# Optimization experiments

Hardware: AMD Instinct MI355X
Metric: run time of the kernel (lower is better)

The kernel has to match this reference:

```python
import jax, jax.numpy as jnp
import numpy as np

B, Nq, C, H = 1, 300, 256, 8
h, w = 32, 32
HW = h * w
HID = 512  # rpe_hidden_dim
HD = C // H


def setup_inputs() -> dict:
    key = jax.random.key(0)
    ks = jax.random.split(key, 16)
    s = 0.02
    inp = {
        "raw_query": jax.random.normal(ks[0], (B, Nq, C), jnp.float32),
        "query_pos": jax.random.normal(ks[1], (B, Nq, C), jnp.float32),
        "reference_points": jax.random.uniform(ks[2], (B, Nq, 2), jnp.float32),
        "raw_src": jax.random.normal(ks[3], (B, HW, C), jnp.float32),
        "src_pos_embed": jax.random.normal(ks[4], (B, HW, C), jnp.float32),
        "Wq": jax.random.normal(ks[5], (C, C), jnp.float32) * s,
        "bq": jnp.zeros((C,), jnp.float32),
        "Wk": jax.random.normal(ks[6], (C, C), jnp.float32) * s,
        "bk": jnp.zeros((C,), jnp.float32),
        "Wv": jax.random.normal(ks[7], (C, C), jnp.float32) * s,
        "bv": jnp.zeros((C,), jnp.float32),
        "Wo": jax.random.normal(ks[8], (C, C), jnp.float32) * s,
        "bo": jnp.zeros((C,), jnp.float32),
        "W1": jax.random.normal(ks[9], (HID, 2), jnp.float32),   # cpb MLP layer 1
        "b1": jnp.zeros((HID,), jnp.float32),
        "W2": jax.random.normal(ks[10], (H, HID), jnp.float32) * s,  # cpb MLP layer 2 (no bias)
        "input_spatial_shapes": np.array([[h, w]], dtype=np.int64),
    }
    return inp


def _key_positions(hh, ww):
    ys = (jnp.arange(hh, dtype=jnp.float32) + 0.5) / hh
    xs = (jnp.arange(ww, dtype=jnp.float32) + 0.5) / ww
    yy, xx = jnp.meshgrid(ys, xs, indexing="ij")  # row-major: idx = y*w + x
    return jnp.stack([xx.ravel(), yy.ravel()], axis=-1)  # [HW, 2] (x, y)


def reference(raw_query, query_pos, reference_points, raw_src, src_pos_embed,
              Wq, bq, Wk, bk, Wv, bv, Wo, bo, W1, b1, W2, input_spatial_shapes):
    hh, ww = int(input_spatial_shapes[0, 0]), int(input_spatial_shapes[0, 1])
    scale = HD ** (-0.5)
    queries = raw_query + query_pos                      # [B,Nq,C]
    memory = raw_src + src_pos_embed                     # [B,HW,C]

    q = (queries @ Wq.T + bq).reshape(B, Nq, H, HD)
    k = (memory @ Wk.T + bk).reshape(B, hh * ww, H, HD)
    v = (memory @ Wv.T + bv).reshape(B, hh * ww, H, HD)

    logits = jnp.einsum("bqhd,bkhd->bhqk", q, k) * scale  # [B,H,Nq,HW]

    key_pos = _key_positions(hh, ww)                      # [HW,2]
    delta = reference_points[:, :, None, :] - key_pos[None, None]  # [B,Nq,HW,2]
    hid = jax.nn.relu(jnp.einsum("bqkc,hc->bqkh", delta, W1) + b1)  # [B,Nq,HW,HID]
    bias = jnp.einsum("bqkf,hf->bhqk", hid, W2)           # [B,H,Nq,HW]

    attn = jax.nn.softmax(logits + bias, axis=-1)
    out = jnp.einsum("bhqk,bkhd->bqhd", attn, v).reshape(B, Nq, C)
    return out @ Wo.T + bo
```

## Files before the change

### kernel.cpp

```cpp
#include <hip/hip_runtime.h>
#include <hip/hip_bf16.h>
#include <stdint.h>

#define NQ   300
#define CDIM 256
#define NH   8
#define HD   32
#define HWK  1024
#define HIDD 512

typedef __attribute__((ext_vector_type(8))) short short8;
typedef __attribute__((ext_vector_type(4))) float f32x4;

#define QB_OFF   0
#define KB_OFF   153600
#define VT_OFF   677888
#define PO_OFF   1202176
#define PL_OFF   2430976

__device__ __forceinline__ short sw_bf16(float x){
  union { float f; uint32_t u; } c; c.f = x;
  uint32_t u = c.u;
  u += 0x7fffu + ((u >> 16) & 1u);
  return (short)(u >> 16);
}

__device__ __forceinline__ uint32_t pk_bf16(float a, float b){
  __hip_bfloat162 h = __float22bfloat162_rn(make_float2(a, b));
  uint32_t u; __builtin_memcpy(&u, &h, 4);
  return u;
}

__global__ __launch_bounds__(256) void proj_kernel(
    const float* __restrict__ rq, const float* __restrict__ qp,
    const float* __restrict__ rs, const float* __restrict__ spe,
    const float* __restrict__ Wq, const float* __restrict__ bq,
    const float* __restrict__ Wk, const float* __restrict__ bk,
    const float* __restrict__ Wv, const float* __restrict__ bv,
    const float* __restrict__ Wo, const float* __restrict__ bo,
    char* __restrict__ ws, float* __restrict__ dout, int final_mode)
{
  int bxid = blockIdx.x;
  int tile = bxid >> 1, half = bxid & 1;
  const float *in1, *in2, *W, *bias;
  int r0, M, mode;
  const float* po = (const float*)(ws + PO_OFF);
  const float* pl = (const float*)(ws + PL_OFF);
  if (final_mode){
    in1 = po; in2 = nullptr; W = Wo; bias = bo;
    r0 = tile*16; M = NQ; mode = 3;
  } else if (tile < 19){
    in1 = rq; in2 = qp; W = Wq; bias = bq; r0 = tile*16; M = NQ; mode = 0;
  } else if (tile < 83){
    in1 = rs; in2 = spe; W = Wk; bias = bk; r0 = (tile-19)*16; M = HWK; mode = 1;
  } else {
    in1 = rs; in2 = spe; W = Wv; bias = bv; r0 = (tile-83)*16; M = HWK; mode = 2;
  }
  __shared__ __align__(16) float At[32][20];
  __shared__ float Wl[32][129];
  __shared__ float linv[16][8];
  int tid = threadIdx.x;
  int n_loc = tid & 127;
  int rg = tid >> 7;
  int n = half*128 + n_loc;
  float acc[8];
  float bv_ = bias[n];
  #pragma unroll
  for (int i=0;i<8;i++) acc[i] = bv_;

  if (mode == 3 && tid < 128){
    int r = tid >> 3, hh = tid & 7;
    int gr = r0 + r; if (gr >= M) gr = M - 1;
    float s = pl[(0*NQ+gr)*NH+hh] + pl[(1*NQ+gr)*NH+hh]
            + pl[(2*NQ+gr)*NH+hh] + pl[(3*NQ+gr)*NH+hh];
    linv[r][hh] = 1.0f / s;
  }

  for (int c0 = 0; c0 < CDIM; c0 += 32){
    __syncthreads();
    for (int e = tid; e < 512; e += 256){
      int r = e >> 5, c = e & 31;
      int gr = r0 + r; if (gr >= M) gr = M - 1;
      float v;
      if (mode == 3){
        int cc = c0 + c;
        v = po[(size_t)(0*NQ+gr)*CDIM + cc] + po[(size_t)(1*NQ+gr)*CDIM + cc]
          + po[(size_t)(2*NQ+gr)*CDIM + cc] + po[(size_t)(3*NQ+gr)*CDIM + cc];
        v *= linv[r][c0 >> 5];
      } else {
        v = in1[gr*CDIM + c0 + c];
        if (in2) v += in2[gr*CDIM + c0 + c];
      }
      At[c][r] = v;
    }
    for (int e = tid; e < 4096; e += 256){
      int c = e & 31, nn = e >> 5;
      Wl[c][nn] = W[(half*128 + nn)*CDIM + c0 + c];
    }
    __syncthreads();
    #pragma unroll
    for (int c = 0; c < 32; c++){
      float w = Wl[c][n_loc];
      const float4* ap = (const float4*)&At[c][rg*8];
      float4 a0 = ap[0], a1 = ap[1];
      acc[0] = fmaf(a0.x, w, acc[0]);
      acc[1] = fmaf(a0.y, w, acc[1]);
      acc[2] = fmaf(a0.z, w, acc[2]);
      acc[3] = fmaf(a0.w, w, acc[3]);
      acc[4] = fmaf(a1.x, w, acc[4]);
      acc[5] = fmaf(a1.y, w, acc[5]);
      acc[6] = fmaf(a1.z, w, acc[6]);
      acc[7] = fmaf(a1.w, w, acc[7]);
    }
  }

  if (mode == 0){
    short* qb = (short*)(ws + QB_OFF);
    const float s = 0.17677669529663687f;
    #pragma unroll
    for (int i=0;i<8;i++){
      int gr = r0 + rg*8 + i;
      if (gr < M) qb[gr*CDIM + n] = sw_bf16(acc[i]*s);
    }
  } else if (mode == 1){
    short* kb = (short*)(ws + KB_OFF);
    int h = n >> 5, d = n & 31;
    #pragma unroll
    for (int i=0;i<8;i++){
      int gr = r0 + rg*8 + i;
      if (gr < M) kb[((size_t)h*HWK + gr)*HD + d] = sw_bf16(acc[i]);
    }
  } else if (mode == 2){
    short* vt = (short*)(ws + VT_OFF);
    union { short8 s; uint32_t u[4]; } p;
    #pragma unroll
    for (int i=0;i<4;i++) p.u[i] = pk_bf16(acc[2*i], acc[2*i+1]);
    *(short8*)(vt + n*HWK + r0 + rg*8) = p.s;
  } else {
    #pragma unroll
    for (int i=0;i<8;i++){
      int gr = r0 + rg*8 + i;
      if (gr < M) dout[gr*CDIM + n] = acc[i];
    }
  }
}

__global__ __launch_bounds__(256) void fused_kernel(
    const float* __restrict__ refp, const float* __restrict__ W1,
    const float* __restrict__ b1, const float* __restrict__ W2,
    const short* __restrict__ qb, const short* __restrict__ kb,
    const short* __restrict__ vt, float* __restrict__ po,
    float* __restrict__ pl)
{
  int bid = blockIdx.x;
  int q = bid >> 2, kr = bid & 3;
  int tid = threadIdx.x, wave = tid >> 6, lane = tid & 63;
  int n = lane & 15, qd = lane >> 4;

  __shared__ __align__(16) float av[HIDD];
  __shared__ __align__(16) float wxs[HIDD];
  __shared__ __align__(16) float wys[HIDD];
  __shared__ __align__(16) short w2l[NH][520];
  __shared__ __align__(16) short pb[NH][264];
  __shared__ __align__(16) float part[4][NH][32];
  __shared__ float lsum[4][NH];

  float rx = refp[2*q], ry = refp[2*q+1];
  for (int f = tid; f < HIDD; f += 256){
    float2 w = ((const float2*)W1)[f];
    wxs[f] = w.x; wys[f] = w.y;
    av[f] = fmaf(w.x, rx, fmaf(w.y, ry, b1[f]));
  }
  for (int e = tid; e < 512; e += 256){
    int r = e >> 6, oc = e & 63;
    const float4* p4 = (const float4*)(W2 + r*HIDD + oc*8);
    float4 x0 = p4[0], x1 = p4[1];
    union { short8 s; uint32_t u[4]; } t;
    t.u[0] = pk_bf16(x0.x, x0.y);
    t.u[1] = pk_bf16(x0.z, x0.w);
    t.u[2] = pk_bf16(x1.x, x1.y);
    t.u[3] = pk_bf16(x1.z, x1.w);
    *(short8*)&w2l[r][oc*8] = t.s;
  }
  short8 qfrag;
  if (n < NH) qfrag = *(const short8*)(qb + q*CDIM + n*HD + qd*8);
  else { short8 z = {0,0,0,0,0,0,0,0}; qfrag = z; }
  __syncthreads();

  const int kbase = kr*256 + wave*64;

  f32x4 acc[4];
  #pragma unroll
  for (int t = 0; t < 4; t++){
    int k0 = kbase + t*16;
    f32x4 sel = {0.f,0.f,0.f,0.f};
    #pragma unroll
    for (int h = 0; h < NH; h++){
      short8 af = *(const short8*)(kb + ((size_t)h*HWK + k0 + n)*HD + qd*8);
      f32x4 d = {0.f,0.f,0.f,0.f};
      d = __builtin_amdgcn_mfma_f32_16x16x32_bf16(af, qfrag, d, 0, 0, 0);
      if (n == h) sel = d;
    }
    acc[t] = sel;
  }

  float kxA = ((float)n + 0.5f) * (1.0f/32.0f);
  float kxB = ((float)n + 16.5f) * (1.0f/32.0f);
  float kyA = ((float)(kbase >> 5) + 0.5f) * (1.0f/32.0f);
  float kyB = kyA + (1.0f/32.0f);
  #pragma unroll 2
  for (int kc = 0; kc < 16; kc++){
    int f0 = kc*32 + qd*8;
    f32x4 a0  = *(const f32x4*)&av[f0],  a1  = *(const f32x4*)&av[f0+4];
    f32x4 wx0 = *(const f32x4*)&wxs[f0], wx1 = *(const f32x4*)&wxs[f0+4];
    f32x4 wy0 = *(const f32x4*)&wys[f0], wy1 = *(const f32x4*)&wys[f0+4];
    short8 bfr = *(const short8*)&w2l[n & 7][kc*32 + qd*8];
    f32x4 tA0, tA1, tB0, tB1;
    #pragma unroll
    for (int j = 0; j < 4; j++){
      tA0[j] = fmaf(-wy0[j], kyA, a0[j]);
      tA1[j] = fmaf(-wy1[j], kyA, a1[j]);
      tB0[j] = fmaf(-wy0[j], kyB, a0[j]);
      tB1[j] = fmaf(-wy1[j], kyB, a1[j]);
    }
    #pragma unroll
    for (int t = 0; t < 4; t++){
      const f32x4& u0 = (t < 2) ? tA0 : tB0;
      const f32x4& u1 = (t < 2) ? tA1 : tB1;
      float kx = (t & 1) ? kxB : kxA;
      float e0 = fmaxf(fmaf(-wx0[0], kx, u0[0]), 0.f);
      float e1 = fmaxf(fmaf(-wx0[1], kx, u0[1]), 0.f);
      float e2 = fmaxf(fmaf(-wx0[2], kx, u0[2]), 0.f);
      float e3 = fmaxf(fmaf(-wx0[3], kx, u0[3]), 0.f);
      float e4 = fmaxf(fmaf(-wx1[0], kx, u1[0]), 0.f);
      float e5 = fmaxf(fmaf(-wx1[1], kx, u1[1]), 0.f);
      float e6 = fmaxf(fmaf(-wx1[2], kx, u1[2]), 0.f);
      float e7 = fmaxf(fmaf(-wx1[3], kx, u1[3]), 0.f);
      union { short8 s; uint32_t u[4]; } r;
      r.u[0] = pk_bf16(e0, e1);
      r.u[1] = pk_bf16(e2, e3);
      r.u[2] = pk_bf16(e4, e5);
      r.u[3] = pk_bf16(e6, e7);
      acc[t] = __builtin_amdgcn_mfma_f32_16x16x32_bf16(r.s, bfr, acc[t], 0, 0, 0);
    }
  }

  float lacc = 0.f;
  #pragma unroll
  for (int t = 0; t < 4; t++){
    float e0 = __expf(acc[t][0]);
    float e1 = __expf(acc[t][1]);
    float e2 = __expf(acc[t][2]);
    float e3 = __expf(acc[t][3]);
    if (n < NH){
      uint2 p2;
      p2.x = pk_bf16(e0, e1);
      p2.y = pk_bf16(e2, e3);
      *(uint2*)&pb[n][wave*64 + t*16 + qd*4] = p2;
    }
    float s = e0 + e1 + e2 + e3;
    s += __shfl_xor(s, 16);
    s += __shfl_xor(s, 32);
    lacc += s;
  }
  if (lane < NH) lsum[wave][lane] = lacc;

  #pragma unroll
  for (int h = 0; h < NH; h++){
    f32x4 o0 = {0.f,0.f,0.f,0.f}, o1 = {0.f,0.f,0.f,0.f};
    #pragma unroll
    for (int i = 0; i < 2; i++){
      int kl = wave*64 + i*32 + qd*8;
      short8 pa = *(const short8*)&pb[h][kl];
      short8 v0 = *(const short8*)(vt + ((size_t)(h*HD +      n))*HWK + kr*256 + kl);
      short8 v1 = *(const short8*)(vt + ((size_t)(h*HD + 16 + n))*HWK + kr*256 + kl);
      o0 = __builtin_amdgcn_mfma_f32_16x16x32_bf16(pa, v0, o0, 0, 0, 0);
      o1 = __builtin_amdgcn_mfma_f32_16x16x32_bf16(pa, v1, o1, 0, 0, 0);
    }
    if (qd == 0){
      part[wave][h][n]      = o0[0];
      part[wave][h][16 + n] = o1[0];
    }
  }
  __syncthreads();

  {
    int h = tid >> 5, d = tid & 31;
    float s = part[0][h][d] + part[1][h][d] + part[2][h][d] + part[3][h][d];
    po[((size_t)kr*NQ + q)*CDIM + tid] = s;
    if (tid < NH)
      pl[((size_t)kr*NQ + q)*NH + tid] =
          lsum[0][tid] + lsum[1][tid] + lsum[2][tid] + lsum[3][tid];
  }
}

extern "C" void kernel_launch(void* const* d_in, const int* in_sizes, int n_in,
                              void* d_out, int out_size, void* d_ws, size_t ws_size,
                              hipStream_t stream)
{
  const float* rq  = (const float*)d_in[0];
  const float* qp  = (const float*)d_in[1];
  const float* rp  = (const float*)d_in[2];
  const float* rs  = (const float*)d_in[3];
  const float* spe = (const float*)d_in[4];
  const float* Wq  = (const float*)d_in[5];
  const float* bq  = (const float*)d_in[6];
  const float* Wk  = (const float*)d_in[7];
  const float* bk  = (const float*)d_in[8];
  const float* Wv  = (const float*)d_in[9];
  const float* bv  = (const float*)d_in[10];
  const float* Wo  = (const float*)d_in[11];
  const float* bo  = (const float*)d_in[12];
  const float* W1  = (const float*)d_in[13];
  const float* b1  = (const float*)d_in[14];
  const float* W2  = (const float*)d_in[15];
  char* ws = (char*)d_ws;
  float* dout = (float*)d_out;

  proj_kernel<<<294, 256, 0, stream>>>(rq, qp, rs, spe, Wq, bq, Wk, bk,
      Wv, bv, Wo, bo, ws, dout, 0);
  fused_kernel<<<1200, 256, 0, stream>>>(rp, W1, b1, W2,
      (const short*)(ws + QB_OFF), (const short*)(ws + KB_OFF),
      (const short*)(ws + VT_OFF), (float*)(ws + PO_OFF),
      (float*)(ws + PL_OFF));
  proj_kernel<<<38, 256, 0, stream>>>(rq, qp, rs, spe, Wq, bq, Wk, bk,
      Wv, bv, Wo, bo, ws, dout, 1);
}
```

Measured before the change: 171.7 us.

## Split fused attention into eight key chunks per query with per-row hidden precompute

Result: no change. 171.5 us (-0.1%).

```diff
diff --git a/kernel.cpp b/kernel.cpp
--- a/kernel.cpp
+++ b/kernel.cpp
@@ -16,7 +16,7 @@
 #define KB_OFF   153600
 #define VT_OFF   677888
 #define PO_OFF   1202176
-#define PL_OFF   2430976
+#define PL_OFF   3659776
 
 __device__ __forceinline__ short sw_bf16(float x){
   union { float f; uint32_t u; } c; c.f = x;
@@ -71,8 +71,9 @@
   if (mode == 3 && tid < 128){
     int r = tid >> 3, hh = tid & 7;
     int gr = r0 + r; if (gr >= M) gr = M - 1;
-    float s = pl[(0*NQ+gr)*NH+hh] + pl[(1*NQ+gr)*NH+hh]
-            + pl[(2*NQ+gr)*NH+hh] + pl[(3*NQ+gr)*NH+hh];
+    float s = 0.f;
+    #pragma unroll
+    for (int p = 0; p < 8; p++) s += pl[((size_t)p*NQ+gr)*NH+hh];
     linv[r][hh] = 1.0f / s;
   }
 
@@ -84,8 +85,9 @@
       float v;
       if (mode == 3){
         int cc = c0 + c;
-        v = po[(size_t)(0*NQ+gr)*CDIM + cc] + po[(size_t)(1*NQ+gr)*CDIM + cc]
-          + po[(size_t)(2*NQ+gr)*CDIM + cc] + po[(size_t)(3*NQ+gr)*CDIM + cc];
+        v = 0.f;
+        #pragma unroll
+        for (int p = 0; p < 8; p++) v += po[(size_t)(p*NQ+gr)*CDIM + cc];
         v *= linv[r][c0 >> 5];
       } else {
         v = in1[gr*CDIM + c0 + c];
@@ -145,7 +147,7 @@
   }
 }
 
-__global__ __launch_bounds__(256) void fused_kernel(
+__global__ __launch_bounds__(256, 4) void fused_kernel(
     const float* __restrict__ refp, const float* __restrict__ W1,
     const float* __restrict__ b1, const float* __restrict__ W2,
     const short* __restrict__ qb, const short* __restrict__ kb,
@@ -153,23 +155,27 @@
     float* __restrict__ pl)
 {
   int bid = blockIdx.x;
-  int q = bid >> 2, kr = bid & 3;
+  int q = bid >> 3, kr = bid & 7;
   int tid = threadIdx.x, wave = tid >> 6, lane = tid & 63;
   int n = lane & 15, qd = lane >> 4;
 
-  __shared__ __align__(16) float av[HIDD];
   __shared__ __align__(16) float wxs[HIDD];
-  __shared__ __align__(16) float wys[HIDD];
+  __shared__ __align__(16) float c1s[4][HIDD];
   __shared__ __align__(16) short w2l[NH][520];
-  __shared__ __align__(16) short pb[NH][264];
+  __shared__ __align__(16) short pb[NH][136];
   __shared__ __align__(16) float part[4][NH][32];
   __shared__ float lsum[4][NH];
 
   float rx = refp[2*q], ry = refp[2*q+1];
   for (int f = tid; f < HIDD; f += 256){
     float2 w = ((const float2*)W1)[f];
-    wxs[f] = w.x; wys[f] = w.y;
-    av[f] = fmaf(w.x, rx, fmaf(w.y, ry, b1[f]));
+    wxs[f] = w.x;
+    float a = fmaf(w.x, rx, fmaf(w.y, ry, b1[f]));
+    #pragma unroll
+    for (int r = 0; r < 4; r++){
+      float ky = ((float)(kr*4 + r) + 0.5f) * (1.0f/32.0f);
+      c1s[r][f] = fmaf(-w.y, ky, a);
+    }
   }
   for (int e = tid; e < 512; e += 256){
     int r = e >> 6, oc = e & 63;
@@ -185,57 +191,50 @@
   short8 qfrag;
   if (n < NH) qfrag = *(const short8*)(qb + q*CDIM + n*HD + qd*8);
   else { short8 z = {0,0,0,0,0,0,0,0}; qfrag = z; }
+  short8 qm[NH];
+  #pragma unroll
+  for (int h = 0; h < NH; h++){
+    short8 z = {0,0,0,0,0,0,0,0};
+    qm[h] = (n == h) ? qfrag : z;
+  }
   __syncthreads();
 
-  const int kbase = kr*256 + wave*64;
-
-  f32x4 acc[4];
-  #pragma unroll
-  for (int t = 0; t < 4; t++){
+  const int kyrow = kr*4 + wave;
+  const int kbase = kyrow * 32;
+
+  f32x4 acc[2];
+  #pragma unroll
+  for (int t = 0; t < 2; t++){
     int k0 = kbase + t*16;
-    f32x4 sel = {0.f,0.f,0.f,0.f};
+    f32x4 d = {0.f,0.f,0.f,0.f};
     #pragma unroll
     for (int h = 0; h < NH; h++){
       short8 af = *(const short8*)(kb + ((size_t)h*HWK + k0 + n)*HD + qd*8);
-      f32x4 d = {0.f,0.f,0.f,0.f};
-      d = __builtin_amdgcn_mfma_f32_16x16x32_bf16(af, qfrag, d, 0, 0, 0);
-      if (n == h) sel = d;
-    }
-    acc[t] = sel;
+      d = __builtin_amdgcn_mfma_f32_16x16x32_bf16(af, qm[h], d, 0, 0, 0);
+    }
+    acc[t] = d;
   }
 
   float kxA = ((float)n + 0.5f) * (1.0f/32.0f);
   float kxB = ((float)n + 16.5f) * (1.0f/32.0f);
-  float kyA = ((float)(kbase >> 5) + 0.5f) * (1.0f/32.0f);
-  float kyB = kyA + (1.0f/32.0f);
-  #pragma unroll 2
+  const float* c1r = &c1s[wave][0];
+  #pragma unroll 4
   for (int kc = 0; kc < 16; kc++){
     int f0 = kc*32 + qd*8;
-    f32x4 a0  = *(const f32x4*)&av[f0],  a1  = *(const f32x4*)&av[f0+4];
+    f32x4 c0 = *(const f32x4*)(c1r + f0), c1v = *(const f32x4*)(c1r + f0 + 4);
     f32x4 wx0 = *(const f32x4*)&wxs[f0], wx1 = *(const f32x4*)&wxs[f0+4];
-    f32x4 wy0 = *(const f32x4*)&wys[f0], wy1 = *(const f32x4*)&wys[f0+4];
     short8 bfr = *(const short8*)&w2l[n & 7][kc*32 + qd*8];
-    f32x4 tA0, tA1, tB0, tB1;
-    #pragma unroll
-    for (int j = 0; j < 4; j++){
-      tA0[j] = fmaf(-wy0[j], kyA, a0[j]);
-      tA1[j] = fmaf(-wy1[j], kyA, a1[j]);
-      tB0[j] = fmaf(-wy0[j], kyB, a0[j]);
-      tB1[j] = fmaf(-wy1[j], kyB, a1[j]);
-    }
-    #pragma unroll
-    for (int t = 0; t < 4; t++){
-      const f32x4& u0 = (t < 2) ? tA0 : tB0;
-      const f32x4& u1 = (t < 2) ? tA1 : tB1;
-      float kx = (t & 1) ? kxB : kxA;
-      float e0 = fmaxf(fmaf(-wx0[0], kx, u0[0]), 0.f);
-      float e1 = fmaxf(fmaf(-wx0[1], kx, u0[1]), 0.f);
-      float e2 = fmaxf(fmaf(-wx0[2], kx, u0[2]), 0.f);
-      float e3 = fmaxf(fmaf(-wx0[3], kx, u0[3]), 0.f);
-      float e4 = fmaxf(fmaf(-wx1[0], kx, u1[0]), 0.f);
-      float e5 = fmaxf(fmaf(-wx1[1], kx, u1[1]), 0.f);
-      float e6 = fmaxf(fmaf(-wx1[2], kx, u1[2]), 0.f);
-      float e7 = fmaxf(fmaf(-wx1[3], kx, u1[3]), 0.f);
+    #pragma unroll
+    for (int t = 0; t < 2; t++){
+      float kx = t ? kxB : kxA;
+      float e0 = fmaxf(fmaf(-wx0[0], kx, c0[0]), 0.f);
+      float e1 = fmaxf(fmaf(-wx0[1], kx, c0[1]), 0.f);
+      float e2 = fmaxf(fmaf(-wx0[2], kx, c0[2]), 0.f);
+      float e3 = fmaxf(fmaf(-wx0[3], kx, c0[3]), 0.f);
+      float e4 = fmaxf(fmaf(-wx1[0], kx, c1v[0]), 0.f);
+      float e5 = fmaxf(fmaf(-wx1[1], kx, c1v[1]), 0.f);
+      float e6 = fmaxf(fmaf(-wx1[2], kx, c1v[2]), 0.f);
+      float e7 = fmaxf(fmaf(-wx1[3], kx, c1v[3]), 0.f);
       union { short8 s; uint32_t u[4]; } r;
       r.u[0] = pk_bf16(e0, e1);
       r.u[1] = pk_bf16(e2, e3);
@@ -247,7 +246,7 @@
 
   float lacc = 0.f;
   #pragma unroll
-  for (int t = 0; t < 4; t++){
+  for (int t = 0; t < 2; t++){
     float e0 = __expf(acc[t][0]);
     float e1 = __expf(acc[t][1]);
     float e2 = __expf(acc[t][2]);
@@ -256,7 +255,7 @@
       uint2 p2;
       p2.x = pk_bf16(e0, e1);
       p2.y = pk_bf16(e2, e3);
-      *(uint2*)&pb[n][wave*64 + t*16 + qd*4] = p2;
+      *(uint2*)&pb[n][wave*32 + t*16 + qd*4] = p2;
     }
     float s = e0 + e1 + e2 + e3;
     s += __shfl_xor(s, 16);
@@ -267,16 +266,13 @@
 
   #pragma unroll
   for (int h = 0; h < NH; h++){
+    int kl = wave*32 + qd*8;
+    short8 pa = *(const short8*)&pb[h][kl];
+    short8 v0 = *(const short8*)(vt + ((size_t)(h*HD +      n))*HWK + kr*128 + kl);
+    short8 v1 = *(const short8*)(vt + ((size_t)(h*HD + 16 + n))*HWK + kr*128 + kl);
     f32x4 o0 = {0.f,0.f,0.f,0.f}, o1 = {0.f,0.f,0.f,0.f};
-    #pragma unroll
-    for (int i = 0; i < 2; i++){
-      int kl = wave*64 + i*32 + qd*8;
-      short8 pa = *(const short8*)&pb[h][kl];
-      short8 v0 = *(const short8*)(vt + ((size_t)(h*HD +      n))*HWK + kr*256 + kl);
-      short8 v1 = *(const short8*)(vt + ((size_t)(h*HD + 16 + n))*HWK + kr*256 + kl);
-      o0 = __builtin_amdgcn_mfma_f32_16x16x32_bf16(pa, v0, o0, 0, 0, 0);
-      o1 = __builtin_amdgcn_mfma_f32_16x16x32_bf16(pa, v1, o1, 0, 0, 0);
-    }
+    o0 = __builtin_amdgcn_mfma_f32_16x16x32_bf16(pa, v0, o0, 0, 0, 0);
+    o1 = __builtin_amdgcn_mfma_f32_16x16x32_bf16(pa, v1, o1, 0, 0, 0);
     if (qd == 0){
       part[wave][h][n]      = o0[0];
       part[wave][h][16 + n] = o1[0];
@@ -319,7 +315,7 @@
 
   proj_kernel<<<294, 256, 0, stream>>>(rq, qp, rs, spe, Wq, bq, Wk, bk,
       Wv, bv, Wo, bo, ws, dout, 0);
-  fused_kernel<<<1200, 256, 0, stream>>>(rp, W1, b1, W2,
+  fused_kernel<<<2400, 256, 0, stream>>>(rp, W1, b1, W2,
       (const short*)(ws + QB_OFF), (const short*)(ws + KB_OFF),
       (const short*)(ws + VT_OFF), (float*)(ws + PO_OFF),
       (float*)(ws + PL_OFF));
```
